# Optimization experiments

Measured on AMD Instinct MI355X. Metric: run time of the kernel, lower is better.

The kernel has to match this reference:

```python
import jax, jax.numpy as jnp
import numpy as np

B, N, C = 4, 3136, 64
IMG_H = IMG_W = 56
HEADS = 1
TOPK = 8
HID = 4 * C  # mlp_ratio=4.0


def _ln(x, g, b, eps=1e-5):
    m = x.mean(-1, keepdims=True)
    v = ((x - m) ** 2).mean(-1, keepdims=True)
    return (x - m) * jax.lax.rsqrt(v + eps) * g + b


def _conv(x, w, b, pad, groups):
    y = jax.lax.conv_general_dilated(
        x, w, (1, 1), [(pad, pad), (pad, pad)],
        dimension_numbers=('NCHW', 'OIHW', 'NCHW'), feature_group_count=groups)
    return y + b[None, :, None, None]


def setup_inputs() -> dict:
    key = jax.random.key(0)
    ks = jax.random.split(key, 10)
    def rn(k, shp, scale=0.02):
        return jax.random.normal(k, shp, jnp.float32) * scale
    return {
        'x': jax.random.normal(ks[0], (B, N, C), jnp.float32),
        'norm1_g': jnp.ones((C,), jnp.float32), 'norm1_b': jnp.zeros((C,), jnp.float32),
        'wq': rn(ks[1], (C, C)), 'bq': jnp.zeros((C,), jnp.float32),
        'wkv': rn(ks[2], (C, 2 * C)), 'bkv': jnp.zeros((2 * C,), jnp.float32),
        'wproj': rn(ks[3], (C, C)), 'bproj': jnp.zeros((C,), jnp.float32),
        'local_w': rn(ks[4], (C, C // HEADS, 3, 3), 0.05), 'local_b': jnp.zeros((C,), jnp.float32),
        'norm2_g': jnp.ones((C,), jnp.float32), 'norm2_b': jnp.zeros((C,), jnp.float32),
        'w3': rn(ks[5], (HID, 1, 3, 3), 0.05), 'b3': jnp.zeros((HID,), jnp.float32),
        'w5': rn(ks[6], (HID, 1, 5, 5), 0.05), 'b5': jnp.zeros((HID,), jnp.float32),
        'w1': rn(ks[7], (C, 2 * HID, 1, 1), 0.05), 'b1': jnp.zeros((C,), jnp.float32),
        'H': IMG_H, 'W': IMG_W,
    }


def reference(x, norm1_g, norm1_b, wq, bq, wkv, bkv, wproj, bproj,
              local_w, local_b, norm2_g, norm2_b, w3, b3, w5, b5, w1, b1, H, W):
    Bb, Nn, Cc = x.shape
    d = Cc // HEADS
    scale = d ** -0.5
    # --- DynamicSparseAttention (global branch) ---
    xn = _ln(x, norm1_g, norm1_b)
    q = (xn @ wq + bq).reshape(Bb, Nn, HEADS, d).transpose(0, 2, 1, 3)       # bhnd
    kv = (xn @ wkv + bkv).reshape(Bb, Nn, 2, HEADS, d)
    k = kv[:, :, 0].transpose(0, 2, 1, 3)
    v = kv[:, :, 1].transpose(0, 2, 1, 3)
    attn = jnp.einsum('bhnd,bhmd->bhnm', q, k) * scale                        # [B,h,N,N]
    kth = jax.lax.top_k(attn, TOPK)[0][..., -1:]                              # k-th largest per row
    mask = (attn >= kth).astype(attn.dtype)                                   # top-k scatter mask
    p = jax.nn.softmax(attn * mask, axis=-1)                                  # zeros kept (as in torch ref)
    g = jnp.einsum('bhnm,bhmd->bhnd', p, v).transpose(0, 2, 1, 3).reshape(Bb, Nn, Cc)
    g = g @ wproj + bproj
    # --- local conv attention branch ---
    x_img = x.transpose(0, 2, 1).reshape(Bb, Cc, H, W)
    loc = _conv(x_img, local_w, local_b, 1, HEADS).reshape(Bb, Cc, Nn).transpose(0, 2, 1)
    # --- residual 1 (note: norm1 params reused, as in source) ---
    x = x + _ln(g + loc, norm1_g, norm1_b)
    # --- MSFN ---
    xn2 = _ln(x, norm2_g, norm2_b).transpose(0, 2, 1).reshape(Bb, Cc, H, W)
    x3 = _conv(xn2, w3, b3, 1, Cc)   # depthwise 3x3, channel mult 4
    x5 = _conv(xn2, w5, b5, 2, Cc)   # depthwise 5x5, channel mult 4
    m = _conv(jnp.concatenate([x3, x5], axis=1), w1, b1, 0, 1)
    return x + m.reshape(Bb, Cc, Nn).transpose(0, 2, 1)
```

## Files before the change

kernel.cpp:

```cpp
#include <hip/hip_runtime.h>
#include <math.h>

#define Bv 4
#define Nv 3136
#define Cv 64
#define Hh 56
#define Ww 56
#define HIDv 256
#define TOPKv 8
#define TSP 520
#define LCP 584
#define XNP 72

constexpr float SCALE = 0.125f;
constexpr float EPS = 1e-5f;

typedef short bf16x8 __attribute__((ext_vector_type(8)));
typedef float f32x4 __attribute__((ext_vector_type(4)));

#define CSWAP(a, b) { unsigned int _hi = max(a, b); unsigned int _lo = min(a, b); a = _hi; b = _lo; }
#define BITONIC8(T) \
  CSWAP(T[0], T[4]); CSWAP(T[1], T[5]); CSWAP(T[2], T[6]); CSWAP(T[3], T[7]); \
  CSWAP(T[0], T[2]); CSWAP(T[1], T[3]); CSWAP(T[4], T[6]); CSWAP(T[5], T[7]); \
  CSWAP(T[0], T[1]); CSWAP(T[2], T[3]); CSWAP(T[4], T[5]); CSWAP(T[6], T[7]);

__device__ __forceinline__ unsigned short f2bf(float f) {
  unsigned int u = __float_as_uint(f);
  u = (u + 0x7FFFu + ((u >> 16) & 1u)) >> 16;
  return (unsigned short)u;
}
__device__ __forceinline__ float bf2f(unsigned short u) {
  return __uint_as_float(((unsigned int)u) << 16);
}
__device__ __forceinline__ unsigned int pack2(float a, float b) {
  return (unsigned int)f2bf(a) | ((unsigned int)f2bf(b) << 16);
}

__device__ __forceinline__ unsigned int packScore(float s, int j) {
  unsigned int b = __float_as_uint(s);
  unsigned int m = b ^ ((b & 0x80000000u) ? 0xFFFFFFFFu : 0x80000000u);
  return (m & 0xFFFFF000u) | (unsigned int)j;
}
__device__ __forceinline__ float unpackScore(unsigned int p) {
  unsigned int m = p & 0xFFFFF000u;
  unsigned int b = (m & 0x80000000u) ? (m ^ 0x80000000u) : ~m;
  return __uint_as_float(b);
}

__global__ void k_transpose(const float* __restrict__ w1, const float* __restrict__ lw,
                            const float* __restrict__ w3, const float* __restrict__ w5,
                            const float* __restrict__ wq, const float* __restrict__ wkv,
                            const float* __restrict__ bq, const float* __restrict__ bkv,
                            const float* __restrict__ wproj,
                            unsigned short* __restrict__ w1bf, unsigned short* __restrict__ lwb,
                            float* __restrict__ w3t, float* __restrict__ w5t,
                            unsigned short* __restrict__ wqkvt, float* __restrict__ qkvb,
                            unsigned short* __restrict__ wprojt) {
  int p = blockIdx.x * 256 + threadIdx.x;
  if (p < 64 * 512) w1bf[p] = f2bf(w1[p]);
  if (p < 64 * 576) {
    int co = p / 576, k = p % 576;
    int tap = k >> 6, ci = k & 63;
    lwb[p] = f2bf(lw[co * 576 + ci * 9 + tap]);
  }
  if (p < 36 * 64) {
    int cin = p & 63, tm = p >> 6;
    int tap = tm >> 2, m = tm & 3;
    w3t[p] = w3[(cin * 4 + m) * 9 + tap];
  }
  if (p < 100 * 64) {
    int cin = p & 63, tm = p >> 6;
    int tap = tm >> 2, m = tm & 3;
    w5t[p] = w5[(cin * 4 + m) * 25 + tap];
  }
  if (p < 192 * 64) {
    int o = p >> 6, i = p & 63;
    float v = (o < 64) ? wq[i * 64 + o] : wkv[i * 128 + (o - 64)];
    wqkvt[p] = f2bf(v);
  }
  if (p < 192) qkvb[p] = (p < 64) ? bq[p] : bkv[p - 64];
  if (p < 64 * 64) {
    int o = p >> 6, i = p & 63;
    wprojt[p] = f2bf(wproj[i * 64 + o]);
  }
}

__global__ __launch_bounds__(256) void k_ln_qkv(
    const float* __restrict__ x, const float* __restrict__ g1, const float* __restrict__ b1,
    const unsigned short* __restrict__ wqkvt, const float* __restrict__ qkvb,
    unsigned short* __restrict__ q16, unsigned short* __restrict__ k16,
    float* __restrict__ vo, unsigned short* __restrict__ x16) {
  __shared__ __align__(16) unsigned short xnS[64 * XNP];
  int t = threadIdx.x;
  int w = t >> 6, l = t & 63;
  int n = l & 15, q = l >> 4;
  int tokL = w * 16 + n;
  size_t tok = (size_t)blockIdx.x * 64 + tokL;
  int ch0 = q * 16;
  float v[16];
  const float* xp = &x[tok * 64 + ch0];
#pragma unroll
  for (int i = 0; i < 4; ++i) *(float4*)&v[i * 4] = *(const float4*)&xp[i * 4];
  {
    unsigned int pk[8];
#pragma unroll
    for (int i = 0; i < 8; ++i) pk[i] = pack2(v[2 * i], v[2 * i + 1]);
    *(uint4*)&x16[tok * 64 + ch0] = *(uint4*)&pk[0];
    *(uint4*)&x16[tok * 64 + ch0 + 8] = *(uint4*)&pk[4];
  }
  float s = 0.f, s2 = 0.f;
#pragma unroll
  for (int i = 0; i < 16; ++i) { s += v[i]; s2 += v[i] * v[i]; }
  s += __shfl_xor(s, 16, 64); s += __shfl_xor(s, 32, 64);
  s2 += __shfl_xor(s2, 16, 64); s2 += __shfl_xor(s2, 32, 64);
  float m = s * (1.f / 64.f);
  float var = s2 * (1.f / 64.f) - m * m;
  float rs = rsqrtf(var + EPS);
  {
    unsigned int* xnU = (unsigned int*)xnS;
    unsigned int pk[8];
#pragma unroll
    for (int i = 0; i < 8; ++i) {
      float a = (v[2 * i] - m) * rs * g1[ch0 + 2 * i] + b1[ch0 + 2 * i];
      float b_ = (v[2 * i + 1] - m) * rs * g1[ch0 + 2 * i + 1] + b1[ch0 + 2 * i + 1];
      pk[i] = pack2(a, b_);
    }
#pragma unroll
    for (int i = 0; i < 8; ++i) xnU[(tokL * XNP + ch0) / 2 + i] = pk[i];
  }
  __syncthreads();

  const bf16x8 a0 = *(const bf16x8*)&xnS[(w * 16 + n) * XNP + q * 8];
  const bf16x8 a1 = *(const bf16x8*)&xnS[(w * 16 + n) * XNP + 32 + q * 8];
  size_t tbase = (size_t)blockIdx.x * 64 + w * 16;
#pragma unroll
  for (int j = 0; j < 4; ++j) {
    const unsigned short* wr = &wqkvt[(size_t)(j * 16 + n) * 64];
    bf16x8 b0 = *(const bf16x8*)&wr[q * 8];
    bf16x8 b1_ = *(const bf16x8*)&wr[32 + q * 8];
    f32x4 acc = {0.f, 0.f, 0.f, 0.f};
    acc = __builtin_amdgcn_mfma_f32_16x16x32_bf16(a0, b0, acc, 0, 0, 0);
    acc = __builtin_amdgcn_mfma_f32_16x16x32_bf16(a1, b1_, acc, 0, 0, 0);
    float bias = qkvb[j * 16 + n];
#pragma unroll
    for (int r = 0; r < 4; ++r)
      q16[(tbase + q * 4 + r) * 64 + j * 16 + n] = f2bf(acc[r] + bias);
  }
#pragma unroll
  for (int j = 0; j < 4; ++j) {
    const unsigned short* wr = &wqkvt[(size_t)((j + 4) * 16 + n) * 64];
    bf16x8 b0 = *(const bf16x8*)&wr[q * 8];
    bf16x8 b1_ = *(const bf16x8*)&wr[32 + q * 8];
    f32x4 acc = {0.f, 0.f, 0.f, 0.f};
    acc = __builtin_amdgcn_mfma_f32_16x16x32_bf16(a0, b0, acc, 0, 0, 0);
    acc = __builtin_amdgcn_mfma_f32_16x16x32_bf16(a1, b1_, acc, 0, 0, 0);
    float bias = qkvb[64 + j * 16 + n];
#pragma unroll
    for (int r = 0; r < 4; ++r)
      k16[(tbase + q * 4 + r) * 64 + j * 16 + n] = f2bf(acc[r] + bias);
  }
#pragma unroll
  for (int j = 0; j < 4; ++j) {
    const unsigned short* wr = &wqkvt[(size_t)((j + 8) * 16 + n) * 64];
    bf16x8 b0 = *(const bf16x8*)&wr[q * 8];
    bf16x8 b1_ = *(const bf16x8*)&wr[32 + q * 8];
    f32x4 acc = {0.f, 0.f, 0.f, 0.f};
    acc = __builtin_amdgcn_mfma_f32_16x16x32_bf16(a0, b0, acc, 0, 0, 0);
    acc = __builtin_amdgcn_mfma_f32_16x16x32_bf16(a1, b1_, acc, 0, 0, 0);
    float bias = qkvb[128 + j * 16 + n];
#pragma unroll
    for (int r = 0; r < 4; ++r)
      vo[(tbase + q * 4 + r) * 64 + j * 16 + n] = acc[r] + bias;
  }
}

__global__ void k_sumv(const float* __restrict__ v, float* __restrict__ sumv) {
  __shared__ float part[4][64];
  int b = blockIdx.x / 49, slice = blockIdx.x % 49;
  int w = threadIdx.x >> 6, c = threadIdx.x & 63;
  float acc = 0.0f;
  int base = b * Nv + slice * 64 + w * 16;
#pragma unroll
  for (int n = 0; n < 16; ++n) acc += v[(size_t)(base + n) * 64 + c];
  part[w][c] = acc;
  __syncthreads();
  if (threadIdx.x < 64) {
    float s = part[0][c] + part[1][c] + part[2][c] + part[3][c];
    atomicAdd(&sumv[b * 64 + c], s);
  }
}

__global__ __launch_bounds__(256) void k_attn_topk(
    const unsigned short* __restrict__ q16, const unsigned short* __restrict__ k16,
    unsigned int* __restrict__ top8out) {
  __shared__ unsigned int candLDS[16][4][9];
  int bid = blockIdx.x;
  int half = bid & 1;
  int lin = bid >> 1;
  int b = lin / 196, tile = lin % 196;
  int qbase = b * Nv + tile * 16;
  size_t bN = (size_t)b * Nv;
  int t = threadIdx.x;
  int w = t >> 6, lane = t & 63;
  int qcol = lane & 15, quad = lane >> 4;

  const bf16x8 qf0 = *(const bf16x8*)&q16[((size_t)(qbase + qcol)) * 64 + quad * 8];
  const bf16x8 qf1 = *(const bf16x8*)&q16[((size_t)(qbase + qcol)) * 64 + 32 + quad * 8];

  unsigned int t8[8];
  unsigned int PACKNEG = packScore(-1e30f, 0);
#pragma unroll
  for (int u = 0; u < 8; ++u) t8[u] = PACKNEG;
  float thrRaw = -3.0e38f;

  int chBeg = half ? 24 : 0;
  int chEnd = half ? 49 : 24;
  int keyRow = w * 16 + qcol;
  bf16x8 kf0 = *(const bf16x8*)&k16[(bN + chBeg * 64 + keyRow) * 64 + quad * 8];
  bf16x8 kf1 = *(const bf16x8*)&k16[(bN + chBeg * 64 + keyRow) * 64 + 32 + quad * 8];

  for (int ch = chBeg; ch < chEnd; ++ch) {
    bf16x8 c0 = kf0, c1 = kf1;
    if (ch + 1 < chEnd) {
      kf0 = *(const bf16x8*)&k16[(bN + (ch + 1) * 64 + keyRow) * 64 + quad * 8];
      kf1 = *(const bf16x8*)&k16[(bN + (ch + 1) * 64 + keyRow) * 64 + 32 + quad * 8];
    }
    f32x4 acc = {0.f, 0.f, 0.f, 0.f};
    acc = __builtin_amdgcn_mfma_f32_16x16x32_bf16(c0, qf0, acc, 0, 0, 0);
    acc = __builtin_amdgcn_mfma_f32_16x16x32_bf16(c1, qf1, acc, 0, 0, 0);
    float m01 = fmaxf(acc[0], acc[1]);
    float m23 = fmaxf(acc[2], acc[3]);
    if (fmaxf(m01, m23) > thrRaw) {
      int jb = ch * 64 + w * 16 + quad * 4;
      unsigned int p0 = packScore(acc[0] * SCALE, jb + 0);
      unsigned int p1 = packScore(acc[1] * SCALE, jb + 1);
      unsigned int p2 = packScore(acc[2] * SCALE, jb + 2);
      unsigned int p3 = packScore(acc[3] * SCALE, jb + 3);
      CSWAP(p0, p1); CSWAP(p2, p3); CSWAP(p0, p2); CSWAP(p1, p3); CSWAP(p1, p2);
      t8[4] = max(t8[4], p3);
      t8[5] = max(t8[5], p2);
      t8[6] = max(t8[6], p1);
      t8[7] = max(t8[7], p0);
      BITONIC8(t8);
      thrRaw = unpackScore(t8[7]) * 8.0f;
    }
  }

#pragma unroll
  for (int step = 16; step <= 32; step <<= 1) {
    unsigned int o[8];
#pragma unroll
    for (int i = 0; i < 8; ++i) o[i] = (unsigned int)__shfl_xor((int)t8[i], step, 64);
    unsigned int nw[8];
#pragma unroll
    for (int i = 0; i < 8; ++i) nw[i] = max(t8[i], o[7 - i]);
#pragma unroll
    for (int i = 0; i < 8; ++i) t8[i] = nw[i];
    BITONIC8(t8);
  }
  if (quad == 0) {
#pragma unroll
    for (int i = 0; i < 8; ++i) candLDS[qcol][w][i] = t8[i];
  }
  __syncthreads();

  if (t < 16) {
    int r = t;
    int p0 = 0, p1 = 0, p2 = 0, p3 = 0;
    size_t obase = ((size_t)(bN + tile * 16 + r)) * 16 + half * 8;
#pragma unroll
    for (int u = 0; u < 8; ++u) {
      unsigned int c0 = (p0 < 8) ? candLDS[r][0][p0] : 0u;
      unsigned int c1 = (p1 < 8) ? candLDS[r][1][p1] : 0u;
      unsigned int c2 = (p2 < 8) ? candLDS[r][2][p2] : 0u;
      unsigned int c3 = (p3 < 8) ? candLDS[r][3][p3] : 0u;
      unsigned int best = c0;
      int bw = 0;
      if (c1 > best) { best = c1; bw = 1; }
      if (c2 > best) { best = c2; bw = 2; }
      if (c3 > best) { best = c3; bw = 3; }
      p0 += (bw == 0); p1 += (bw == 1); p2 += (bw == 2); p3 += (bw == 3);
      top8out[obase + u] = best;
    }
  }
}

__global__ __launch_bounds__(256) void k_attn_out(
    const unsigned int* __restrict__ top8, const float* __restrict__ vg,
    const float* __restrict__ sumv, float* __restrict__ gout) {
  __shared__ float kwS[16][8];
  __shared__ int kidxS[16][8];
  __shared__ float invZS[16];
  int b = blockIdx.x / 196, tile = blockIdx.x % 196;
  int qbase = b * Nv + tile * 16;
  size_t bN = (size_t)b * Nv;
  int t = threadIdx.x;
  if (t < 16) {
    size_t base = (size_t)(qbase + t) * 16;
    unsigned int A[8], Bb[8];
#pragma unroll
    for (int i = 0; i < 8; ++i) A[i] = top8[base + i];
#pragma unroll
    for (int i = 0; i < 8; ++i) Bb[i] = top8[base + 8 + i];
#pragma unroll
    for (int i = 0; i < 8; ++i) A[i] = max(A[i], Bb[7 - i]);
    BITONIC8(A);
    float Z = (float)(Nv - TOPKv);
#pragma unroll
    for (int u = 0; u < 8; ++u) {
      float s = unpackScore(A[u]);
      float e = __expf(s);
      kwS[t][u] = e - 1.0f;
      kidxS[t][u] = (int)(A[u] & 0xFFFu);
      Z += e;
    }
    invZS[t] = 1.0f / Z;
  }
  __syncthreads();
  int c = t & 63, rg = t >> 6;
#pragma unroll 1
  for (int rr = 0; rr < 4; ++rr) {
    int r = rg * 4 + rr;
    float acc = sumv[b * 64 + c];
#pragma unroll
    for (int u = 0; u < 8; ++u)
      acc += kwS[r][u] * vg[(bN + kidxS[r][u]) * 64 + c];
    gout[(size_t)(qbase + r) * 64 + c] = acc * invZS[r];
  }
}

__global__ __launch_bounds__(256) void k_locconv(
    const unsigned short* __restrict__ x16, const unsigned short* __restrict__ lwb,
    const float* __restrict__ lb, float* __restrict__ loc) {
  __shared__ __align__(16) unsigned short im[16 * LCP];
  int bid = blockIdx.x;
  int b = bid / 196, rem = bid % 196;
  int th = rem / 7, tw = rem % 7;
  int h0 = th * 2, w0 = tw * 8;
  size_t bN = (size_t)b * Nv;
  int t = threadIdx.x;
  for (int p = t; p < 1152; p += 256) {
    int sub = p & 7, s = p >> 3;
    int tok = s / 9, tap = s % 9;
    int tr = tok >> 3, tc = tok & 7;
    int dh = tap / 3, dw = tap % 3;
    int gh = h0 + tr - 1 + dh, gw = w0 + tc - 1 + dw;
    bf16x8 v = {};
    if (gh >= 0 && gh < Hh && gw >= 0 && gw < Ww)
      v = *(const bf16x8*)&x16[(bN + gh * Ww + gw) * 64 + sub * 8];
    *(bf16x8*)&im[tok * LCP + tap * 64 + sub * 8] = v;
  }
  __syncthreads();
  int wv = t >> 6, lane = t & 63;
  int n16 = lane & 15, quad = lane >> 4;
  const unsigned short* wrow = &lwb[(size_t)(wv * 16 + n16) * 576];
  f32x4 acc = {0.f, 0.f, 0.f, 0.f};
#pragma unroll 6
  for (int kk = 0; kk < 18; ++kk) {
    bf16x8 af = *(const bf16x8*)&im[n16 * LCP + kk * 32 + quad * 8];
    bf16x8 bfr = *(const bf16x8*)&wrow[kk * 32 + quad * 8];
    acc = __builtin_amdgcn_mfma_f32_16x16x32_bf16(af, bfr, acc, 0, 0, 0);
  }
  float bias = lb[wv * 16 + n16];
#pragma unroll
  for (int r = 0; r < 4; ++r) {
    int tok = quad * 4 + r;
    int trr = tok >> 3, tcc = tok & 7;
    size_t idx = (bN + (size_t)(h0 + trr) * Ww + w0 + tcc) * 64 + wv * 16 + n16;
    loc[idx] = acc[r] + bias;
  }
}

__global__ __launch_bounds__(256) void k_proj_res(
    const float* __restrict__ x, const float* __restrict__ gin,
    const float* __restrict__ loc,
    const unsigned short* __restrict__ wprojt, const float* __restrict__ bproj,
    const float* __restrict__ g1, const float* __restrict__ b1,
    const float* __restrict__ g2, const float* __restrict__ b2,
    float* __restrict__ x2, unsigned short* __restrict__ xn2b) {
  __shared__ __align__(16) unsigned short gS[64 * XNP];
  __shared__ float yS[64 * 66];
  int t = threadIdx.x;
  int w = t >> 6, l = t & 63;
  int n = l & 15, q = l >> 4;
  int tokL = w * 16 + n;
  size_t tok = (size_t)blockIdx.x * 64 + tokL;
  int ch0 = q * 16;
  {
    float gv[16];
    const float* gp = &gin[tok * 64 + ch0];
#pragma unroll
    for (int i = 0; i < 4; ++i) *(float4*)&gv[i * 4] = *(const float4*)&gp[i * 4];
    unsigned int* gU = (unsigned int*)gS;
#pragma unroll
    for (int i = 0; i < 8; ++i)
      gU[(tokL * XNP + ch0) / 2 + i] = pack2(gv[2 * i], gv[2 * i + 1]);
  }
  __syncthreads();
  {
    const bf16x8 a0 = *(const bf16x8*)&gS[(w * 16 + n) * XNP + q * 8];
    const bf16x8 a1 = *(const bf16x8*)&gS[(w * 16 + n) * XNP + 32 + q * 8];
    size_t tbase = (size_t)blockIdx.x * 64 + w * 16;
#pragma unroll
    for (int j = 0; j < 4; ++j) {
      const unsigned short* wr = &wprojt[(size_t)(j * 16 + n) * 64];
      bf16x8 b0 = *(const bf16x8*)&wr[q * 8];
      bf16x8 b1_ = *(const bf16x8*)&wr[32 + q * 8];
      f32x4 acc = {0.f, 0.f, 0.f, 0.f};
      acc = __builtin_amdgcn_mfma_f32_16x16x32_bf16(a0, b0, acc, 0, 0, 0);
      acc = __builtin_amdgcn_mfma_f32_16x16x32_bf16(a1, b1_, acc, 0, 0, 0);
      float bias = bproj[j * 16 + n];
#pragma unroll
      for (int r = 0; r < 4; ++r) {
        size_t idx = (tbase + q * 4 + r) * 64 + j * 16 + n;
        yS[(w * 16 + q * 4 + r) * 66 + j * 16 + n] = acc[r] + bias + loc[idx];
      }
    }
  }
  __syncthreads();
  float y[16];
#pragma unroll
  for (int i = 0; i < 4; ++i) *(float4*)&y[i * 4] = *(const float4*)&yS[tokL * 66 + ch0 + i * 4];
  float s = 0.f, s2 = 0.f;
#pragma unroll
  for (int i = 0; i < 16; ++i) { s += y[i]; s2 += y[i] * y[i]; }
  s += __shfl_xor(s, 16, 64); s += __shfl_xor(s, 32, 64);
  s2 += __shfl_xor(s2, 16, 64); s2 += __shfl_xor(s2, 32, 64);
  float m1 = s * (1.f / 64.f);
  float rs1 = rsqrtf(s2 * (1.f / 64.f) - m1 * m1 + EPS);
  float xv[16];
  const float* xp = &x[tok * 64 + ch0];
#pragma unroll
  for (int i = 0; i < 4; ++i) *(float4*)&xv[i * 4] = *(const float4*)&xp[i * 4];
  float x2v[16];
  float t_s = 0.f, t_s2 = 0.f;
#pragma unroll
  for (int i = 0; i < 16; ++i) {
    float t1 = (y[i] - m1) * rs1 * g1[ch0 + i] + b1[ch0 + i];
    x2v[i] = xv[i] + t1;
    t_s += x2v[i]; t_s2 += x2v[i] * x2v[i];
  }
  t_s += __shfl_xor(t_s, 16, 64); t_s += __shfl_xor(t_s, 32, 64);
  t_s2 += __shfl_xor(t_s2, 16, 64); t_s2 += __shfl_xor(t_s2, 32, 64);
  float m2 = t_s * (1.f / 64.f);
  float rs2 = rsqrtf(t_s2 * (1.f / 64.f) - m2 * m2 + EPS);
  float* x2p = &x2[tok * 64 + ch0];
#pragma unroll
  for (int i = 0; i < 4; ++i) *(float4*)&x2p[i * 4] = *(const float4*)&x2v[i * 4];
  unsigned int pk[8];
#pragma unroll
  for (int i = 0; i < 8; ++i) {
    float a = (x2v[2 * i] - m2) * rs2 * g2[ch0 + 2 * i] + b2[ch0 + 2 * i];
    float b_ = (x2v[2 * i + 1] - m2) * rs2 * g2[ch0 + 2 * i + 1] + b2[ch0 + 2 * i + 1];
    pk[i] = pack2(a, b_);
  }
  *(uint4*)&xn2b[tok * 64 + ch0] = *(uint4*)&pk[0];
  *(uint4*)&xn2b[tok * 64 + ch0 + 8] = *(uint4*)&pk[4];
}

__global__ __launch_bounds__(256) void k_msfn(
    const unsigned short* __restrict__ xn2b, const float* __restrict__ x2,
    const float* __restrict__ w3t, const float* __restrict__ b3,
    const float* __restrict__ w5t, const float* __restrict__ b5,
    const unsigned short* __restrict__ w1bf, const float* __restrict__ b1,
    float* __restrict__ out) {
  __shared__ __align__(16) unsigned short xtS[6 * 12 * 64];
  __shared__ __align__(16) unsigned short tsS[16 * TSP];

  int bid = blockIdx.x;
  int b = bid / 196;
  int rem = bid % 196;
  int th = rem / 7, tw = rem % 7;
  int h0 = th * 2, w0 = tw * 8;
  size_t bN = (size_t)b * Nv;
  int t = threadIdx.x;

  unsigned int* xtU = (unsigned int*)xtS;
  for (int p = t; p < 6 * 12 * 32; p += 256) {
    int cp = p & 31, rc = p >> 5;
    int r = rc / 12, cc = rc % 12;
    int gh = h0 - 2 + r, gw = w0 - 2 + cc;
    unsigned int v = 0;
    if (gh >= 0 && gh < Hh && gw >= 0 && gw < Ww)
      v = *(const unsigned int*)&xn2b[(bN + gh * Ww + gw) * 64 + cp * 2];
    xtU[rc * 32 + cp] = v;
  }
  __syncthreads();

  int cin = t & 63, tg = t >> 6;
  int tr = tg >> 1, tc0 = (tg & 1) * 4;
  float win[5][8];
#pragma unroll
  for (int r = 0; r < 5; ++r)
#pragma unroll
    for (int c = 0; c < 8; ++c)
      win[r][c] = bf2f(xtS[((tr + r) * 12 + tc0 + c) * 64 + cin]);

  unsigned int* tsU = (unsigned int*)tsS;
#pragma unroll 1
  for (int m2 = 0; m2 < 4; m2 += 2) {
    float a3[2][9], a5[2][25], bb3[2], bb5[2];
#pragma unroll
    for (int mm = 0; mm < 2; ++mm) {
      int m = m2 + mm;
#pragma unroll
      for (int tap = 0; tap < 9; ++tap) a3[mm][tap] = w3t[(tap * 4 + m) * 64 + cin];
#pragma unroll
      for (int tap = 0; tap < 25; ++tap) a5[mm][tap] = w5t[(tap * 4 + m) * 64 + cin];
      bb3[mm] = b3[cin * 4 + m];
      bb5[mm] = b5[cin * 4 + m];
    }
#pragma unroll
    for (int tk = 0; tk < 4; ++tk) {
      int tok = tg * 4 + tk;
      unsigned int p3 = 0, p5 = 0;
#pragma unroll
      for (int mm = 0; mm < 2; ++mm) {
        float acc3 = bb3[mm];
#pragma unroll
        for (int kh = 0; kh < 3; ++kh)
#pragma unroll
          for (int kw2 = 0; kw2 < 3; ++kw2)
            acc3 += win[1 + kh][tk + 1 + kw2] * a3[mm][kh * 3 + kw2];
        float acc5 = bb5[mm];
#pragma unroll
        for (int kh = 0; kh < 5; ++kh)
#pragma unroll
          for (int kw2 = 0; kw2 < 5; ++kw2)
            acc5 += win[kh][tk + kw2] * a5[mm][kh * 5 + kw2];
        p3 |= (unsigned int)f2bf(acc3) << (16 * mm);
        p5 |= (unsigned int)f2bf(acc5) << (16 * mm);
      }
      tsU[(tok * TSP + cin * 4 + m2) >> 1] = p3;
      tsU[(tok * TSP + 256 + cin * 4 + m2) >> 1] = p5;
    }
  }
  __syncthreads();

  int wv = tg, lane = t & 63;
  int n16 = lane & 15, quad = lane >> 4;
  const unsigned short* wrow = &w1bf[(size_t)(wv * 16 + n16) * 512];
  f32x4 acc = {0.f, 0.f, 0.f, 0.f};
#pragma unroll 4
  for (int kk = 0; kk < 16; ++kk) {
    bf16x8 af = *(const bf16x8*)&tsS[n16 * TSP + kk * 32 + quad * 8];
    bf16x8 bfr = *(const bf16x8*)&wrow[kk * 32 + quad * 8];
    acc = __builtin_amdgcn_mfma_f32_16x16x32_bf16(af, bfr, acc, 0, 0, 0);
  }
  float bias = b1[wv * 16 + n16];
#pragma unroll
  for (int r = 0; r < 4; ++r) {
    int tok = quad * 4 + r;
    int trr = tok >> 3, tcc = tok & 7;
    size_t idx = (bN + (size_t)(h0 + trr) * Ww + w0 + tcc) * 64 + wv * 16 + n16;
    out[idx] = x2[idx] + acc[r] + bias;
  }
}

extern "C" void kernel_launch(void* const* d_in, const int* in_sizes, int n_in,
                              void* d_out, int out_size, void* d_ws, size_t ws_size,
                              hipStream_t stream) {
  const float* x = (const float*)d_in[0];
  const float* n1g = (const float*)d_in[1];
  const float* n1b = (const float*)d_in[2];
  const float* wq = (const float*)d_in[3];
  const float* bq = (const float*)d_in[4];
  const float* wkv = (const float*)d_in[5];
  const float* bkv = (const float*)d_in[6];
  const float* wproj = (const float*)d_in[7];
  const float* bproj = (const float*)d_in[8];
  const float* lw = (const float*)d_in[9];
  const float* lb = (const float*)d_in[10];
  const float* n2g = (const float*)d_in[11];
  const float* n2b = (const float*)d_in[12];
  const float* w3 = (const float*)d_in[13];
  const float* b3 = (const float*)d_in[14];
  const float* w5 = (const float*)d_in[15];
  const float* b5 = (const float*)d_in[16];
  const float* w1 = (const float*)d_in[17];
  const float* b1 = (const float*)d_in[18];
  float* out = (float*)d_out;

  float* ws = (float*)d_ws;
  const size_t TOK = (size_t)Bv * Nv * Cv;
  float* vb = ws;
  float* gb = vb + TOK;
  float* sumv = gb + TOK;
  float* loc = sumv + 256;
  float* x2 = loc + TOK;
  float* w3t = x2 + TOK;
  float* w5t = w3t + 2304;
  float* qkvb = w5t + 6400;
  unsigned short* q16 = (unsigned short*)(qkvb + 192);
  unsigned short* k16 = q16 + TOK;
  unsigned short* xn2b = k16 + TOK;
  unsigned short* x16 = xn2b + TOK;
  unsigned short* w1bf = x16 + TOK;
  unsigned short* lwb = w1bf + 64 * 512;
  unsigned short* wqkvt = lwb + 64 * 576;
  unsigned short* wprojt = wqkvt + 192 * 64;
  unsigned int* top8ws = (unsigned int*)(wprojt + 64 * 64 + 64);

  k_transpose<<<144, 256, 0, stream>>>(w1, lw, w3, w5, wq, wkv, bq, bkv, wproj,
                                       w1bf, lwb, w3t, w5t, wqkvt, qkvb, wprojt);
  k_ln_qkv<<<Bv * Nv / 64, 256, 0, stream>>>(x, n1g, n1b, wqkvt, qkvb, q16, k16, vb, x16);
  hipMemsetAsync(sumv, 0, 256 * sizeof(float), stream);
  k_sumv<<<Bv * 49, 256, 0, stream>>>(vb, sumv);
  k_attn_topk<<<Bv * 196 * 2, 256, 0, stream>>>(q16, k16, top8ws);
  k_locconv<<<Bv * 196, 256, 0, stream>>>(x16, lwb, lb, loc);
  k_attn_out<<<Bv * 196, 256, 0, stream>>>(top8ws, vb, sumv, gb);
  k_proj_res<<<Bv * Nv / 64, 256, 0, stream>>>(x, gb, loc, wprojt, bproj, n1g, n1b, n2g, n2b, x2, xn2b);
  k_msfn<<<Bv * 196, 256, 0, stream>>>(xn2b, x2, w3t, b3, w5t, b5, w1bf, b1, out);
}
```

Measured before the change: 197.4 us.

## Fuse sumV into QKV, merge attn-out with projection, split top-k into quarters

The V column sum is folded into the LN+QKV kernel through shuffles and atomics, which removes the separate k_sumv pass over V. The LN+QKV kernel now works on 16-token tiles with one output column group per wave, giving four times as many blocks. The top-k scan is split across four key-range blocks per query tile instead of two, and the merge of the four partial top-8 lists moves into a new kernel that also does the projection, residual and both layernorms. This drops the g intermediate buffer and one launch, at the cost of more atomics and a larger partial top-k buffer.

```diff
diff --git a/kernel.cpp b/kernel.cpp
--- a/kernel.cpp
+++ b/kernel.cpp
@@ -89,104 +89,85 @@
     const float* __restrict__ x, const float* __restrict__ g1, const float* __restrict__ b1,
     const unsigned short* __restrict__ wqkvt, const float* __restrict__ qkvb,
     unsigned short* __restrict__ q16, unsigned short* __restrict__ k16,
-    float* __restrict__ vo, unsigned short* __restrict__ x16) {
-  __shared__ __align__(16) unsigned short xnS[64 * XNP];
+    float* __restrict__ vo, unsigned short* __restrict__ x16,
+    float* __restrict__ sumv) {
+  __shared__ __align__(16) unsigned short xnS[16 * XNP];
+  int bid = blockIdx.x;
+  int b = bid / 196, tile = bid % 196;
+  size_t tok0 = (size_t)b * Nv + tile * 16;
   int t = threadIdx.x;
   int w = t >> 6, l = t & 63;
+  int tokL = t >> 4;
+  int ch0 = (t & 15) * 4;
+  size_t tok = tok0 + tokL;
+  float v[4];
+  *(float4*)v = *(const float4*)&x[tok * 64 + ch0];
+  {
+    unsigned int pk[2] = {pack2(v[0], v[1]), pack2(v[2], v[3])};
+    *(uint2*)&x16[tok * 64 + ch0] = *(uint2*)pk;
+  }
+  float s = v[0] + v[1] + v[2] + v[3];
+  float s2 = v[0] * v[0] + v[1] * v[1] + v[2] * v[2] + v[3] * v[3];
+#pragma unroll
+  for (int off = 1; off <= 8; off <<= 1) {
+    s += __shfl_xor(s, off, 64);
+    s2 += __shfl_xor(s2, off, 64);
+  }
+  float m = s * (1.f / 64.f);
+  float rs = rsqrtf(s2 * (1.f / 64.f) - m * m + EPS);
+  {
+    unsigned int pk[2];
+    float a0_ = (v[0] - m) * rs * g1[ch0] + b1[ch0];
+    float a1_ = (v[1] - m) * rs * g1[ch0 + 1] + b1[ch0 + 1];
+    float a2_ = (v[2] - m) * rs * g1[ch0 + 2] + b1[ch0 + 2];
+    float a3_ = (v[3] - m) * rs * g1[ch0 + 3] + b1[ch0 + 3];
+    pk[0] = pack2(a0_, a1_);
+    pk[1] = pack2(a2_, a3_);
+    *(uint2*)&xnS[tokL * XNP + ch0] = *(uint2*)pk;
+  }
+  __syncthreads();
   int n = l & 15, q = l >> 4;
-  int tokL = w * 16 + n;
-  size_t tok = (size_t)blockIdx.x * 64 + tokL;
-  int ch0 = q * 16;
-  float v[16];
-  const float* xp = &x[tok * 64 + ch0];
-#pragma unroll
-  for (int i = 0; i < 4; ++i) *(float4*)&v[i * 4] = *(const float4*)&xp[i * 4];
-  {
-    unsigned int pk[8];
-#pragma unroll
-    for (int i = 0; i < 8; ++i) pk[i] = pack2(v[2 * i], v[2 * i + 1]);
-    *(uint4*)&x16[tok * 64 + ch0] = *(uint4*)&pk[0];
-    *(uint4*)&x16[tok * 64 + ch0 + 8] = *(uint4*)&pk[4];
-  }
-  float s = 0.f, s2 = 0.f;
-#pragma unroll
-  for (int i = 0; i < 16; ++i) { s += v[i]; s2 += v[i] * v[i]; }
-  s += __shfl_xor(s, 16, 64); s += __shfl_xor(s, 32, 64);
-  s2 += __shfl_xor(s2, 16, 64); s2 += __shfl_xor(s2, 32, 64);
-  float m = s * (1.f / 64.f);
-  float var = s2 * (1.f / 64.f) - m * m;
-  float rs = rsqrtf(var + EPS);
-  {
-    unsigned int* xnU = (unsigned int*)xnS;
-    unsigned int pk[8];
-#pragma unroll
-    for (int i = 0; i < 8; ++i) {
-      float a = (v[2 * i] - m) * rs * g1[ch0 + 2 * i] + b1[ch0 + 2 * i];
-      float b_ = (v[2 * i + 1] - m) * rs * g1[ch0 + 2 * i + 1] + b1[ch0 + 2 * i + 1];
-      pk[i] = pack2(a, b_);
-    }
-#pragma unroll
-    for (int i = 0; i < 8; ++i) xnU[(tokL * XNP + ch0) / 2 + i] = pk[i];
-  }
-  __syncthreads();
-
-  const bf16x8 a0 = *(const bf16x8*)&xnS[(w * 16 + n) * XNP + q * 8];
-  const bf16x8 a1 = *(const bf16x8*)&xnS[(w * 16 + n) * XNP + 32 + q * 8];
-  size_t tbase = (size_t)blockIdx.x * 64 + w * 16;
-#pragma unroll
-  for (int j = 0; j < 4; ++j) {
-    const unsigned short* wr = &wqkvt[(size_t)(j * 16 + n) * 64];
+  const bf16x8 a0 = *(const bf16x8*)&xnS[n * XNP + q * 8];
+  const bf16x8 a1 = *(const bf16x8*)&xnS[n * XNP + 32 + q * 8];
+  {
+    const unsigned short* wr = &wqkvt[(size_t)(w * 16 + n) * 64];
     bf16x8 b0 = *(const bf16x8*)&wr[q * 8];
     bf16x8 b1_ = *(const bf16x8*)&wr[32 + q * 8];
     f32x4 acc = {0.f, 0.f, 0.f, 0.f};
     acc = __builtin_amdgcn_mfma_f32_16x16x32_bf16(a0, b0, acc, 0, 0, 0);
     acc = __builtin_amdgcn_mfma_f32_16x16x32_bf16(a1, b1_, acc, 0, 0, 0);
-    float bias = qkvb[j * 16 + n];
+    float bias = qkvb[w * 16 + n];
 #pragma unroll
     for (int r = 0; r < 4; ++r)
-      q16[(tbase + q * 4 + r) * 64 + j * 16 + n] = f2bf(acc[r] + bias);
-  }
-#pragma unroll
-  for (int j = 0; j < 4; ++j) {
-    const unsigned short* wr = &wqkvt[(size_t)((j + 4) * 16 + n) * 64];
+      q16[(tok0 + q * 4 + r) * 64 + w * 16 + n] = f2bf(acc[r] + bias);
+  }
+  {
+    const unsigned short* wr = &wqkvt[(size_t)((w + 4) * 16 + n) * 64];
     bf16x8 b0 = *(const bf16x8*)&wr[q * 8];
     bf16x8 b1_ = *(const bf16x8*)&wr[32 + q * 8];
     f32x4 acc = {0.f, 0.f, 0.f, 0.f};
     acc = __builtin_amdgcn_mfma_f32_16x16x32_bf16(a0, b0, acc, 0, 0, 0);
     acc = __builtin_amdgcn_mfma_f32_16x16x32_bf16(a1, b1_, acc, 0, 0, 0);
-    float bias = qkvb[64 + j * 16 + n];
+    float bias = qkvb[64 + w * 16 + n];
 #pragma unroll
     for (int r = 0; r < 4; ++r)
-      k16[(tbase + q * 4 + r) * 64 + j * 16 + n] = f2bf(acc[r] + bias);
-  }
-#pragma unroll
-  for (int j = 0; j < 4; ++j) {
-    const unsigned short* wr = &wqkvt[(size_t)((j + 8) * 16 + n) * 64];
+      k16[(tok0 + q * 4 + r) * 64 + w * 16 + n] = f2bf(acc[r] + bias);
+  }
+  {
+    const unsigned short* wr = &wqkvt[(size_t)((w + 8) * 16 + n) * 64];
     bf16x8 b0 = *(const bf16x8*)&wr[q * 8];
     bf16x8 b1_ = *(const bf16x8*)&wr[32 + q * 8];
     f32x4 acc = {0.f, 0.f, 0.f, 0.f};
     acc = __builtin_amdgcn_mfma_f32_16x16x32_bf16(a0, b0, acc, 0, 0, 0);
     acc = __builtin_amdgcn_mfma_f32_16x16x32_bf16(a1, b1_, acc, 0, 0, 0);
-    float bias = qkvb[128 + j * 16 + n];
+    float bias = qkvb[128 + w * 16 + n];
+    float vp = acc[0] + acc[1] + acc[2] + acc[3] + 4.0f * bias;
 #pragma unroll
     for (int r = 0; r < 4; ++r)
-      vo[(tbase + q * 4 + r) * 64 + j * 16 + n] = acc[r] + bias;
-  }
-}
-
-__global__ void k_sumv(const float* __restrict__ v, float* __restrict__ sumv) {
-  __shared__ float part[4][64];
-  int b = blockIdx.x / 49, slice = blockIdx.x % 49;
-  int w = threadIdx.x >> 6, c = threadIdx.x & 63;
-  float acc = 0.0f;
-  int base = b * Nv + slice * 64 + w * 16;
-#pragma unroll
-  for (int n = 0; n < 16; ++n) acc += v[(size_t)(base + n) * 64 + c];
-  part[w][c] = acc;
-  __syncthreads();
-  if (threadIdx.x < 64) {
-    float s = part[0][c] + part[1][c] + part[2][c] + part[3][c];
-    atomicAdd(&sumv[b * 64 + c], s);
+      vo[(tok0 + q * 4 + r) * 64 + w * 16 + n] = acc[r] + bias;
+    vp += __shfl_xor(vp, 16, 64);
+    vp += __shfl_xor(vp, 32, 64);
+    if (q == 0) atomicAdd(&sumv[b * 64 + w * 16 + n], vp);
   }
 }
 
@@ -195,8 +176,8 @@
     unsigned int* __restrict__ top8out) {
   __shared__ unsigned int candLDS[16][4][9];
   int bid = blockIdx.x;
-  int half = bid & 1;
-  int lin = bid >> 1;
+  int quarter = bid & 3;
+  int lin = bid >> 2;
   int b = lin / 196, tile = lin % 196;
   int qbase = b * Nv + tile * 16;
   size_t bN = (size_t)b * Nv;
@@ -213,8 +194,8 @@
   for (int u = 0; u < 8; ++u) t8[u] = PACKNEG;
   float thrRaw = -3.0e38f;
 
-  int chBeg = half ? 24 : 0;
-  int chEnd = half ? 49 : 24;
+  int chBeg = (quarter * 49) >> 2;
+  int chEnd = ((quarter + 1) * 49) >> 2;
   int keyRow = w * 16 + qcol;
   bf16x8 kf0 = *(const bf16x8*)&k16[(bN + chBeg * 64 + keyRow) * 64 + quad * 8];
   bf16x8 kf1 = *(const bf16x8*)&k16[(bN + chBeg * 64 + keyRow) * 64 + 32 + quad * 8];
@@ -267,7 +248,7 @@
   if (t < 16) {
     int r = t;
     int p0 = 0, p1 = 0, p2 = 0, p3 = 0;
-    size_t obase = ((size_t)(bN + tile * 16 + r)) * 16 + half * 8;
+    size_t obase = ((size_t)(bN + tile * 16 + r)) * 32 + quarter * 8;
 #pragma unroll
     for (int u = 0; u < 8; ++u) {
       unsigned int c0 = (p0 < 8) ? candLDS[r][0][p0] : 0u;
@@ -285,26 +266,38 @@
   }
 }
 
-__global__ __launch_bounds__(256) void k_attn_out(
+__global__ __launch_bounds__(256) void k_attn_proj(
     const unsigned int* __restrict__ top8, const float* __restrict__ vg,
-    const float* __restrict__ sumv, float* __restrict__ gout) {
+    const float* __restrict__ sumv,
+    const float* __restrict__ x, const float* __restrict__ loc,
+    const unsigned short* __restrict__ wprojt, const float* __restrict__ bproj,
+    const float* __restrict__ g1, const float* __restrict__ b1,
+    const float* __restrict__ g2, const float* __restrict__ b2,
+    float* __restrict__ x2, unsigned short* __restrict__ xn2b) {
   __shared__ float kwS[16][8];
   __shared__ int kidxS[16][8];
   __shared__ float invZS[16];
-  int b = blockIdx.x / 196, tile = blockIdx.x % 196;
-  int qbase = b * Nv + tile * 16;
+  __shared__ __align__(16) unsigned short gS[16 * XNP];
+  __shared__ float yS[16 * 66];
+  int bid = blockIdx.x;
+  int b = bid / 196, tile = bid % 196;
   size_t bN = (size_t)b * Nv;
+  size_t tok0 = bN + tile * 16;
   int t = threadIdx.x;
   if (t < 16) {
-    size_t base = (size_t)(qbase + t) * 16;
-    unsigned int A[8], Bb[8];
+    size_t base = (tok0 + t) * 32;
+    unsigned int A[8];
 #pragma unroll
     for (int i = 0; i < 8; ++i) A[i] = top8[base + i];
 #pragma unroll
-    for (int i = 0; i < 8; ++i) Bb[i] = top8[base + 8 + i];
-#pragma unroll
-    for (int i = 0; i < 8; ++i) A[i] = max(A[i], Bb[7 - i]);
-    BITONIC8(A);
+    for (int h = 1; h < 4; ++h) {
+      unsigned int Bb[8];
+#pragma unroll
+      for (int i = 0; i < 8; ++i) Bb[i] = top8[base + h * 8 + i];
+#pragma unroll
+      for (int i = 0; i < 8; ++i) A[i] = max(A[i], Bb[7 - i]);
+      BITONIC8(A);
+    }
     float Z = (float)(Nv - TOPKv);
 #pragma unroll
     for (int u = 0; u < 8; ++u) {
@@ -317,16 +310,83 @@
     invZS[t] = 1.0f / Z;
   }
   __syncthreads();
-  int c = t & 63, rg = t >> 6;
-#pragma unroll 1
-  for (int rr = 0; rr < 4; ++rr) {
-    int r = rg * 4 + rr;
-    float acc = sumv[b * 64 + c];
-#pragma unroll
-    for (int u = 0; u < 8; ++u)
-      acc += kwS[r][u] * vg[(bN + kidxS[r][u]) * 64 + c];
-    gout[(size_t)(qbase + r) * 64 + c] = acc * invZS[r];
-  }
+  {
+    int c = t & 63, rg = t >> 6;
+    float sv = sumv[b * 64 + c];
+#pragma unroll
+    for (int rr = 0; rr < 4; ++rr) {
+      int tokL = rg * 4 + rr;
+      float acc = sv;
+#pragma unroll
+      for (int u = 0; u < 8; ++u)
+        acc += kwS[tokL][u] * vg[(bN + kidxS[tokL][u]) * 64 + c];
+      gS[tokL * XNP + c] = f2bf(acc * invZS[tokL]);
+    }
+  }
+  __syncthreads();
+  int w = t >> 6, l = t & 63;
+  int n = l & 15, q = l >> 4;
+  {
+    const bf16x8 a0 = *(const bf16x8*)&gS[n * XNP + q * 8];
+    const bf16x8 a1 = *(const bf16x8*)&gS[n * XNP + 32 + q * 8];
+    const unsigned short* wr = &wprojt[(size_t)(w * 16 + n) * 64];
+    bf16x8 b0 = *(const bf16x8*)&wr[q * 8];
+    bf16x8 b1_ = *(const bf16x8*)&wr[32 + q * 8];
+    f32x4 acc = {0.f, 0.f, 0.f, 0.f};
+    acc = __builtin_amdgcn_mfma_f32_16x16x32_bf16(a0, b0, acc, 0, 0, 0);
+    acc = __builtin_amdgcn_mfma_f32_16x16x32_bf16(a1, b1_, acc, 0, 0, 0);
+    float bias = bproj[w * 16 + n];
+#pragma unroll
+    for (int r = 0; r < 4; ++r) {
+      size_t idx = (tok0 + q * 4 + r) * 64 + w * 16 + n;
+      yS[(q * 4 + r) * 66 + w * 16 + n] = acc[r] + bias + loc[idx];
+    }
+  }
+  __syncthreads();
+  int tokL = t >> 4;
+  int ch0 = (t & 15) * 4;
+  size_t tok = tok0 + tokL;
+  float y[4];
+#pragma unroll
+  for (int i = 0; i < 4; ++i) y[i] = yS[tokL * 66 + ch0 + i];
+  float s = y[0] + y[1] + y[2] + y[3];
+  float s2 = y[0] * y[0] + y[1] * y[1] + y[2] * y[2] + y[3] * y[3];
+#pragma unroll
+  for (int off = 1; off <= 8; off <<= 1) {
+    s += __shfl_xor(s, off, 64);
+    s2 += __shfl_xor(s2, off, 64);
+  }
+  float m1 = s * (1.f / 64.f);
+  float rs1 = rsqrtf(s2 * (1.f / 64.f) - m1 * m1 + EPS);
+  float xv[4];
+  *(float4*)xv = *(const float4*)&x[tok * 64 + ch0];
+  float x2v[4];
+  float t_s = 0.f, t_s2 = 0.f;
+#pragma unroll
+  for (int i = 0; i < 4; ++i) {
+    float t1 = (y[i] - m1) * rs1 * g1[ch0 + i] + b1[ch0 + i];
+    x2v[i] = xv[i] + t1;
+    t_s += x2v[i];
+    t_s2 += x2v[i] * x2v[i];
+  }
+#pragma unroll
+  for (int off = 1; off <= 8; off <<= 1) {
+    t_s += __shfl_xor(t_s, off, 64);
+    t_s2 += __shfl_xor(t_s2, off, 64);
+  }
+  float m2 = t_s * (1.f / 64.f);
+  float rs2 = rsqrtf(t_s2 * (1.f / 64.f) - m2 * m2 + EPS);
+  *(float4*)&x2[tok * 64 + ch0] = *(float4*)x2v;
+  unsigned int pk[2];
+  {
+    float a0_ = (x2v[0] - m2) * rs2 * g2[ch0] + b2[ch0];
+    float a1_ = (x2v[1] - m2) * rs2 * g2[ch0 + 1] + b2[ch0 + 1];
+    float a2_ = (x2v[2] - m2) * rs2 * g2[ch0 + 2] + b2[ch0 + 2];
+    float a3_ = (x2v[3] - m2) * rs2 * g2[ch0 + 3] + b2[ch0 + 3];
+    pk[0] = pack2(a0_, a1_);
+    pk[1] = pack2(a2_, a3_);
+  }
+  *(uint2*)&xn2b[tok * 64 + ch0] = *(uint2*)pk;
 }
 
 __global__ __launch_bounds__(256) void k_locconv(
@@ -369,93 +429,6 @@
     size_t idx = (bN + (size_t)(h0 + trr) * Ww + w0 + tcc) * 64 + wv * 16 + n16;
     loc[idx] = acc[r] + bias;
   }
-}
-
-__global__ __launch_bounds__(256) void k_proj_res(
-    const float* __restrict__ x, const float* __restrict__ gin,
-    const float* __restrict__ loc,
-    const unsigned short* __restrict__ wprojt, const float* __restrict__ bproj,
-    const float* __restrict__ g1, const float* __restrict__ b1,
-    const float* __restrict__ g2, const float* __restrict__ b2,
-    float* __restrict__ x2, unsigned short* __restrict__ xn2b) {
-  __shared__ __align__(16) unsigned short gS[64 * XNP];
-  __shared__ float yS[64 * 66];
-  int t = threadIdx.x;
-  int w = t >> 6, l = t & 63;
-  int n = l & 15, q = l >> 4;
-  int tokL = w * 16 + n;
-  size_t tok = (size_t)blockIdx.x * 64 + tokL;
-  int ch0 = q * 16;
-  {
-    float gv[16];
-    const float* gp = &gin[tok * 64 + ch0];
-#pragma unroll
-    for (int i = 0; i < 4; ++i) *(float4*)&gv[i * 4] = *(const float4*)&gp[i * 4];
-    unsigned int* gU = (unsigned int*)gS;
-#pragma unroll
-    for (int i = 0; i < 8; ++i)
-      gU[(tokL * XNP + ch0) / 2 + i] = pack2(gv[2 * i], gv[2 * i + 1]);
-  }
-  __syncthreads();
-  {
-    const bf16x8 a0 = *(const bf16x8*)&gS[(w * 16 + n) * XNP + q * 8];
-    const bf16x8 a1 = *(const bf16x8*)&gS[(w * 16 + n) * XNP + 32 + q * 8];
-    size_t tbase = (size_t)blockIdx.x * 64 + w * 16;
-#pragma unroll
-    for (int j = 0; j < 4; ++j) {
-      const unsigned short* wr = &wprojt[(size_t)(j * 16 + n) * 64];
-      bf16x8 b0 = *(const bf16x8*)&wr[q * 8];
-      bf16x8 b1_ = *(const bf16x8*)&wr[32 + q * 8];
-      f32x4 acc = {0.f, 0.f, 0.f, 0.f};
-      acc = __builtin_amdgcn_mfma_f32_16x16x32_bf16(a0, b0, acc, 0, 0, 0);
-      acc = __builtin_amdgcn_mfma_f32_16x16x32_bf16(a1, b1_, acc, 0, 0, 0);
-      float bias = bproj[j * 16 + n];
-#pragma unroll
-      for (int r = 0; r < 4; ++r) {
-        size_t idx = (tbase + q * 4 + r) * 64 + j * 16 + n;
-        yS[(w * 16 + q * 4 + r) * 66 + j * 16 + n] = acc[r] + bias + loc[idx];
-      }
-    }
-  }
-  __syncthreads();
-  float y[16];
-#pragma unroll
-  for (int i = 0; i < 4; ++i) *(float4*)&y[i * 4] = *(const float4*)&yS[tokL * 66 + ch0 + i * 4];
-  float s = 0.f, s2 = 0.f;
-#pragma unroll
-  for (int i = 0; i < 16; ++i) { s += y[i]; s2 += y[i] * y[i]; }
-  s += __shfl_xor(s, 16, 64); s += __shfl_xor(s, 32, 64);
-  s2 += __shfl_xor(s2, 16, 64); s2 += __shfl_xor(s2, 32, 64);
-  float m1 = s * (1.f / 64.f);
-  float rs1 = rsqrtf(s2 * (1.f / 64.f) - m1 * m1 + EPS);
-  float xv[16];
-  const float* xp = &x[tok * 64 + ch0];
-#pragma unroll
-  for (int i = 0; i < 4; ++i) *(float4*)&xv[i * 4] = *(const float4*)&xp[i * 4];
-  float x2v[16];
-  float t_s = 0.f, t_s2 = 0.f;
-#pragma unroll
-  for (int i = 0; i < 16; ++i) {
-    float t1 = (y[i] - m1) * rs1 * g1[ch0 + i] + b1[ch0 + i];
-    x2v[i] = xv[i] + t1;
-    t_s += x2v[i]; t_s2 += x2v[i] * x2v[i];
-  }
-  t_s += __shfl_xor(t_s, 16, 64); t_s += __shfl_xor(t_s, 32, 64);
-  t_s2 += __shfl_xor(t_s2, 16, 64); t_s2 += __shfl_xor(t_s2, 32, 64);
-  float m2 = t_s * (1.f / 64.f);
-  float rs2 = rsqrtf(t_s2 * (1.f / 64.f) - m2 * m2 + EPS);
-  float* x2p = &x2[tok * 64 + ch0];
-#pragma unroll
-  for (int i = 0; i < 4; ++i) *(float4*)&x2p[i * 4] = *(const float4*)&x2v[i * 4];
-  unsigned int pk[8];
-#pragma unroll
-  for (int i = 0; i < 8; ++i) {
-    float a = (x2v[2 * i] - m2) * rs2 * g2[ch0 + 2 * i] + b2[ch0 + 2 * i];
-    float b_ = (x2v[2 * i + 1] - m2) * rs2 * g2[ch0 + 2 * i + 1] + b2[ch0 + 2 * i + 1];
-    pk[i] = pack2(a, b_);
-  }
-  *(uint4*)&xn2b[tok * 64 + ch0] = *(uint4*)&pk[0];
-  *(uint4*)&xn2b[tok * 64 + ch0 + 8] = *(uint4*)&pk[4];
 }
 
 __global__ __launch_bounds__(256) void k_msfn(
@@ -584,8 +557,7 @@
   float* ws = (float*)d_ws;
   const size_t TOK = (size_t)Bv * Nv * Cv;
   float* vb = ws;
-  float* gb = vb + TOK;
-  float* sumv = gb + TOK;
+  float* sumv = vb + TOK;
   float* loc = sumv + 256;
   float* x2 = loc + TOK;
   float* w3t = x2 + TOK;
@@ -601,14 +573,13 @@
   unsigned short* wprojt = wqkvt + 192 * 64;
   unsigned int* top8ws = (unsigned int*)(wprojt + 64 * 64 + 64);
 
+  hipMemsetAsync(sumv, 0, 256 * sizeof(float), stream);
   k_transpose<<<144, 256, 0, stream>>>(w1, lw, w3, w5, wq, wkv, bq, bkv, wproj,
                                        w1bf, lwb, w3t, w5t, wqkvt, qkvb, wprojt);
-  k_ln_qkv<<<Bv * Nv / 64, 256, 0, stream>>>(x, n1g, n1b, wqkvt, qkvb, q16, k16, vb, x16);
-  hipMemsetAsync(sumv, 0, 256 * sizeof(float), stream);
-  k_sumv<<<Bv * 49, 256, 0, stream>>>(vb, sumv);
-  k_attn_topk<<<Bv * 196 * 2, 256, 0, stream>>>(q16, k16, top8ws);
+  k_ln_qkv<<<Bv * 196, 256, 0, stream>>>(x, n1g, n1b, wqkvt, qkvb, q16, k16, vb, x16, sumv);
+  k_attn_topk<<<Bv * 196 * 4, 256, 0, stream>>>(q16, k16, top8ws);
   k_locconv<<<Bv * 196, 256, 0, stream>>>(x16, lwb, lb, loc);
-  k_attn_out<<<Bv * 196, 256, 0, stream>>>(top8ws, vb, sumv, gb);
-  k_proj_res<<<Bv * Nv / 64, 256, 0, stream>>>(x, gb, loc, wprojt, bproj, n1g, n1b, n2g, n2b, x2, xn2b);
+  k_attn_proj<<<Bv * 196, 256, 0, stream>>>(top8ws, vb, sumv, x, loc, wprojt, bproj,
+                                            n1g, n1b, n2g, n2b, x2, xn2b);
   k_msfn<<<Bv * 196, 256, 0, stream>>>(xn2b, x2, w3t, b3, w5t, b5, w1bf, b1, out);
 }
```

Result: no change. 194.8 us (-1.3%).
